# Optimization experiments

Hardware: AMD Instinct MI355X
Metric: run time of the kernel (lower is better)

Reference implementation:

```python
import jax, jax.numpy as jnp
import numpy as np

B, S, D, H = 2, 2048, 768, 12
E = D // H  # d_head = 64


def setup_inputs() -> dict:
    key = jax.random.key(0)
    ks = jax.random.split(key, 10)
    scale = 1.0 / np.sqrt(D)
    x = jax.random.normal(ks[0], (B, S, D), dtype=jnp.float32)
    # Additive mask, laid out [H*B, S, S] as the torch forward slices per head.
    attn_mask = jnp.zeros((H * B, S, S), dtype=jnp.float32)
    # Per-head projections (math form: q = x @ Wq[h] + bq[h])
    Wq = jax.random.normal(ks[1], (H, D, E), dtype=jnp.float32) * scale
    bq = jax.random.normal(ks[2], (H, E), dtype=jnp.float32) * 0.01
    Wk = jax.random.normal(ks[3], (H, D, E), dtype=jnp.float32) * scale
    bk = jax.random.normal(ks[4], (H, E), dtype=jnp.float32) * 0.01
    Wv = jax.random.normal(ks[5], (H, D, E), dtype=jnp.float32) * scale
    bv = jax.random.normal(ks[6], (H, E), dtype=jnp.float32) * 0.01
    Wo = jax.random.normal(ks[7], (D, D), dtype=jnp.float32) * scale
    bo = jax.random.normal(ks[8], (D,), dtype=jnp.float32) * 0.01
    return {"x": x, "attn_mask": attn_mask, "Wq": Wq, "bq": bq,
            "Wk": Wk, "bk": bk, "Wv": Wv, "bv": bv, "Wo": Wo, "bo": bo}


def reference(x, attn_mask, Wq, bq, Wk, bk, Wv, bv, Wo, bo):
    # x: [B,S,D]; attn_mask: [H*B,S,S]
    q = jnp.einsum('bsd,hde->hbse', x, Wq) + bq[:, None, None, :]
    k = jnp.einsum('bsd,hde->hbse', x, Wk) + bk[:, None, None, :]
    v = jnp.einsum('bsd,hde->hbse', x, Wv) + bv[:, None, None, :]
    mask = attn_mask.reshape(H, B, S, S)
    # NOTE: original code has NO 1/sqrt(d_head) scaling — kept faithful.
    logits = jnp.einsum('hbse,hbte->hbst', q, k) + mask
    w = jax.nn.softmax(logits, axis=-1)  # dropout is identity at eval / p=0
    o = jnp.einsum('hbst,hbte->hbse', w, v)  # [H,B,S,E]
    o = jnp.transpose(o, (1, 2, 0, 3)).reshape(B, S, H * E)  # concat heads
    return o @ Wo + bo
```

## Files before the change

### kernel.cpp

```cpp
#include <hip/hip_runtime.h>
#include <hip/hip_bf16.h>
#include <cmath>

constexpr int Bc  = 2;
constexpr int Sc  = 2048;
constexpr int Dc  = 768;
constexpr int Hc  = 12;
constexpr int Ec  = 64;
constexpr int BSc = Bc * Sc;

typedef _Float16 f16;
typedef __attribute__((ext_vector_type(8)))  _Float16 half8;
typedef __attribute__((ext_vector_type(16))) float    floatx16;

typedef __attribute__((address_space(3))) void       lds_void;
typedef __attribute__((address_space(1))) const void glb_cvoid;


__global__ __launch_bounds__(256) void prep_kernel(
    const float* __restrict__ x,
    const float* __restrict__ Wq, const float* __restrict__ Wk, const float* __restrict__ Wv,
    const float* __restrict__ bq, const float* __restrict__ bk, const float* __restrict__ bv,
    const float* __restrict__ Wo,
    f16* __restrict__ x16, f16* __restrict__ Wt16, f16* __restrict__ Wot16,
    float* __restrict__ bias_cat)
{
    __shared__ __align__(16) float Ts[64][65];
    const int t = threadIdx.x;
    int bid = blockIdx.x;

    if (bid < 1536) {
        const size_t base = (size_t)bid * 2048 + t * 8;
        const float4 v0 = *(const float4*)(x + base);
        const float4 v1 = *(const float4*)(x + base + 4);
        half8 hv;
        hv[0] = (f16)v0.x; hv[1] = (f16)v0.y; hv[2] = (f16)v0.z; hv[3] = (f16)v0.w;
        hv[4] = (f16)v1.x; hv[5] = (f16)v1.y; hv[6] = (f16)v1.z; hv[7] = (f16)v1.w;
        *(half8*)(x16 + base) = hv;
        return;
    }
    bid -= 1536;
    if (bid < 432) {
        const int proj = bid / 144, rem = bid % 144, h = rem / 12, dt = rem % 12;
        const float* W = ((proj == 0) ? Wq : (proj == 1) ? Wk : Wv) + (size_t)h * Dc * Ec;
        const int c = t & 63, rr = t >> 6;
        #pragma unroll
        for (int r0 = 0; r0 < 64; r0 += 4) {
            const int d = rr + r0;
            Ts[d][c] = W[(size_t)(dt * 64 + d) * Ec + c];
        }
        __syncthreads();
        #pragma unroll
        for (int r0 = 0; r0 < 64; r0 += 4) {
            const int e = rr + r0;
            Wt16[(size_t)(proj * 768 + h * 64 + e) * Dc + dt * 64 + c] = (f16)Ts[c][e];
        }
        return;
    }
    bid -= 432;
    if (bid < 144) {
        const int rt = bid / 12, ct = bid % 12;
        const int c = t & 63, rr = t >> 6;
        #pragma unroll
        for (int r0 = 0; r0 < 64; r0 += 4) {
            const int d = rr + r0;
            Ts[d][c] = Wo[(size_t)(rt * 64 + d) * Dc + ct * 64 + c];
        }
        __syncthreads();
        #pragma unroll
        for (int r0 = 0; r0 < 64; r0 += 4) {
            const int e = rr + r0;
            Wot16[(size_t)(ct * 64 + e) * Dc + rt * 64 + c] = (f16)Ts[c][e];
        }
        return;
    }
    bid -= 144;
    {
        const int g = bid * 256 + t;
        if (g < 3 * 768) {
            const int proj = g / 768, idx = g % 768;
            const float* bb = (proj == 0) ? bq : (proj == 1) ? bk : bv;
            bias_cat[g] = bb[idx];
        }
    }
}

__global__ __launch_bounds__(256, 2) void gemm_qkv_kernel(
    const f16* __restrict__ x16, const f16* __restrict__ Wt16,
    const float* __restrict__ bias_cat,
    f16* __restrict__ q16, f16* __restrict__ kswz, f16* __restrict__ vswz)
{
    __shared__ __align__(16) unsigned char smem[34816];
    f16 (*As)[64]  = (f16(*)[64])smem;
    f16 (*Bs)[64]  = (f16(*)[64])(smem + 16384);
    f16 (*Cs)[136] = (f16(*)[136])smem;

    const int t = threadIdx.x;
    const int wave = t >> 6, lane = t & 63;
    const int col = lane & 31, hf = lane >> 5;
    const int wr = wave & 1, wc = wave >> 1;
    const int m0 = blockIdx.x * 128, n0 = blockIdx.y * 128;
    const int lrow = lane >> 3, lseg = lane & 7;

    floatx16 c00, c01, c10, c11;
    #pragma unroll
    for (int i = 0; i < 16; ++i) { c00[i] = 0.f; c01[i] = 0.f; c10[i] = 0.f; c11[i] = 0.f; }

    for (int k0 = 0; k0 < Dc; k0 += 64) {
        #pragma unroll
        for (int i = 0; i < 4; ++i) {
            const int r = wave * 32 + i * 8;
            __builtin_amdgcn_global_load_lds(
                (glb_cvoid*)(x16 + (size_t)(m0 + r + lrow) * Dc + k0 + lseg * 8),
                (lds_void*)&As[r][0], 16, 0, 0);
            __builtin_amdgcn_global_load_lds(
                (glb_cvoid*)(Wt16 + (size_t)(n0 + r + lrow) * Dc + k0 + lseg * 8),
                (lds_void*)&Bs[r][0], 16, 0, 0);
        }
        __syncthreads();
        #pragma unroll
        for (int ks = 0; ks < 4; ++ks) {
            const half8 a0 = *(const half8*)&As[wr * 64 + col][ks * 16 + hf * 8];
            const half8 a1 = *(const half8*)&As[wr * 64 + 32 + col][ks * 16 + hf * 8];
            const half8 b0 = *(const half8*)&Bs[wc * 64 + col][ks * 16 + hf * 8];
            const half8 b1 = *(const half8*)&Bs[wc * 64 + 32 + col][ks * 16 + hf * 8];
            c00 = __builtin_amdgcn_mfma_f32_32x32x16_f16(a0, b0, c00, 0, 0, 0);
            c01 = __builtin_amdgcn_mfma_f32_32x32x16_f16(a0, b1, c01, 0, 0, 0);
            c10 = __builtin_amdgcn_mfma_f32_32x32x16_f16(a1, b0, c10, 0, 0, 0);
            c11 = __builtin_amdgcn_mfma_f32_32x32x16_f16(a1, b1, c11, 0, 0, 0);
        }
        __syncthreads();
    }

    const float bias0 = bias_cat[n0 + wc * 64 + col];
    const float bias1 = bias_cat[n0 + wc * 64 + 32 + col];
    #pragma unroll
    for (int i = 0; i < 16; ++i) {
        const int r = (i & 3) + 8 * (i >> 2) + 4 * hf;
        Cs[wr * 64 + r][wc * 64 + col]           = (f16)(c00[i] + bias0);
        Cs[wr * 64 + r][wc * 64 + 32 + col]      = (f16)(c01[i] + bias1);
        Cs[wr * 64 + 32 + r][wc * 64 + col]      = (f16)(c10[i] + bias0);
        Cs[wr * 64 + 32 + r][wc * 64 + 32 + col] = (f16)(c11[i] + bias1);
    }
    __syncthreads();

    const int proj = n0 / 768;
    const int h0   = (n0 - proj * 768) >> 6;
    const int b    = m0 >> 11;
    const int s_in = m0 & 2047;
    const int kt0  = s_in >> 5;

    if (proj == 0) {
        const int row = t >> 1, seg = t & 1;
        const int h = h0 + seg;
        f16* gp = q16 + ((size_t)(h * Bc + b) * Sc + s_in + row) * Ec;
        #pragma unroll
        for (int j = 0; j < 8; ++j)
            *(half8*)(gp + j * 8) = *(const half8*)&Cs[row][seg * 64 + j * 8];
    } else if (proj == 1) {
        #pragma unroll
        for (int ch = 0; ch < 8; ++ch) {
            const int id = ch * 256 + t;
            const int lane_ = id & 63;
            const int ks  = (id >> 6) & 3;
            const int ktp = (id >> 8) & 3;
            const int seg = (id >> 10) & 1;
            const int colp = lane_ & 31, hfp = lane_ >> 5;
            const int hb = (h0 + seg) * Bc + b;
            const half8 val = *(const half8*)&Cs[ktp * 32 + colp][seg * 64 + ks * 16 + hfp * 8];
            *(half8*)(kswz + ((size_t)((hb * 64 + kt0 + ktp) * 4 + ks) << 9) + lane_ * 8) = val;
        }
    } else {
        #pragma unroll
        for (int ch = 0; ch < 8; ++ch) {
            const int id = ch * 256 + t;
            const int lane_ = id & 63;
            const int ks2 = (id >> 6) & 1;
            const int vh  = (id >> 7) & 1;
            const int ktp = (id >> 8) & 3;
            const int seg = (id >> 10) & 1;
            const int colp = lane_ & 31, hfp = lane_ >> 5;
            const int hb = (h0 + seg) * Bc + b;
            const int e  = vh * 32 + colp;
            half8 val;
            #pragma unroll
            for (int j = 0; j < 8; ++j)
                val[j] = Cs[ktp * 32 + ks2 * 16 + hfp * 8 + j][seg * 64 + e];
            *(half8*)(vswz + ((size_t)(((hb * 64 + kt0 + ktp) * 2 + ks2) * 2 + vh) << 9) + lane_ * 8) = val;
        }
    }
}

__global__ __launch_bounds__(128, 2) void flash_attn_kernel(
    const f16* __restrict__ q16, const f16* __restrict__ kswz,
    const f16* __restrict__ vswz, const float* __restrict__ mask,
    f16* __restrict__ obuf16)
{
    __shared__ __align__(16) float Mall[64 * 128];
    __shared__ _Float16 Plds[2][32][40];

    const int fblk = blockIdx.x;
    const int kk   = fblk >> 3;
    const int hb   = (fblk & 7) + 8 * (kk >> 5);
    const int rb   = kk & 31;
    const int h    = hb >> 1;
    const int b    = hb & 1;

    const int t    = threadIdx.x;
    const int wave = t >> 6;
    const int lane = t & 63;
    const int col  = lane & 31;
    const int hf   = lane >> 5;
    const int row0 = rb * 64 + wave * 32;

    const f16* qb  = q16  + ((size_t)hb * Sc + row0) * Ec;
    const f16* kbz = kswz + ((size_t)hb << 17);
    const f16* vbz = vswz + ((size_t)hb << 17);
    const float* mband = mask + ((size_t)hb * Sc + rb * 64) * Sc;

    half8 qfrag[4];
    #pragma unroll
    for (int ks = 0; ks < 4; ++ks)
        qfrag[ks] = *(const half8*)(qb + (size_t)col * Ec + ks * 16 + hf * 8);

    constexpr int NT = Sc / 32;

    float vmax[16];
    #pragma unroll
    for (int i = 0; i < 16; ++i) vmax[i] = -3e38f;

    half8 kreg[4];
    {
        const f16* kp = kbz + lane * 8;
        #pragma unroll
        for (int ks = 0; ks < 4; ++ks) kreg[ks] = *(const half8*)(kp + (ks << 9));
    }
    #pragma unroll 2
    for (int kt = 0; kt < NT; ++kt) {
        floatx16 c;
        #pragma unroll
        for (int i = 0; i < 16; ++i) c[i] = 0.f;
        #pragma unroll
        for (int ks = 0; ks < 4; ++ks)
            c = __builtin_amdgcn_mfma_f32_32x32x16_f16(qfrag[ks], kreg[ks], c, 0, 0, 0);
        if (kt + 1 < NT) {
            const f16* kp = kbz + ((size_t)(kt + 1) << 11) + lane * 8;
            #pragma unroll
            for (int ks = 0; ks < 4; ++ks) kreg[ks] = *(const half8*)(kp + (ks << 9));
        }
        #pragma unroll
        for (int i = 0; i < 16; ++i) vmax[i] = fmaxf(vmax[i], c[i]);
    }
    float mrow[16];
    #pragma unroll
    for (int i = 0; i < 16; ++i) {
        float v = vmax[i];
        v = fmaxf(v, __shfl_xor(v, 1));
        v = fmaxf(v, __shfl_xor(v, 2));
        v = fmaxf(v, __shfl_xor(v, 4));
        v = fmaxf(v, __shfl_xor(v, 8));
        v = fmaxf(v, __shfl_xor(v, 16));
        mrow[i] = v;
    }

    floatx16 o0, o1;
    float lsum[16];
    #pragma unroll
    for (int i = 0; i < 16; ++i) { o0[i] = 0.f; o1[i] = 0.f; lsum[i] = 0.f; }

    {
        const f16* kp = kbz + lane * 8;
        #pragma unroll
        for (int ks = 0; ks < 4; ++ks) kreg[ks] = *(const half8*)(kp + (ks << 9));
    }

    for (int rd = 0; rd < NT / 4; ++rd) {
        __syncthreads();
        #pragma unroll
        for (int j = 0; j < 16; ++j) {
            const int row = wave * 32 + 2 * j;
            __builtin_amdgcn_global_load_lds(
                (glb_cvoid*)(mband + (size_t)(row + (lane >> 5)) * Sc
                             + rd * 128 + (lane & 31) * 4),
                (lds_void*)&Mall[row * 128], 16, 0, 0);
        }
        __syncthreads();

        #pragma unroll
        for (int s = 0; s < 4; ++s) {
            const int kt = rd * 4 + s;

            const f16* vp = vbz + ((size_t)kt << 11) + lane * 8;
            const half8 va  = *(const half8*)(vp);
            const half8 vb0 = *(const half8*)(vp + (1 << 9));
            const half8 vc  = *(const half8*)(vp + (2 << 9));
            const half8 vd  = *(const half8*)(vp + (3 << 9));

            floatx16 c;
            #pragma unroll
            for (int i = 0; i < 16; ++i) c[i] = 0.f;
            #pragma unroll
            for (int ks = 0; ks < 4; ++ks)
                c = __builtin_amdgcn_mfma_f32_32x32x16_f16(qfrag[ks], kreg[ks], c, 0, 0, 0);

            if (kt + 1 < NT) {
                const f16* kp = kbz + ((size_t)(kt + 1) << 11) + lane * 8;
                #pragma unroll
                for (int ks = 0; ks < 4; ++ks) kreg[ks] = *(const half8*)(kp + (ks << 9));
            }

            #pragma unroll
            for (int i = 0; i < 16; ++i) {
                const int r = (i & 3) + 8 * (i >> 2) + 4 * hf;
                const float m = Mall[(wave * 32 + r) * 128 + s * 32 + col];
                const float p = __expf(c[i] + m - mrow[i]);
                lsum[i] += p;
                Plds[wave][r][col] = (f16)p;
            }
            asm volatile("s_waitcnt lgkmcnt(0)" ::: "memory");

            #pragma unroll
            for (int ks2 = 0; ks2 < 2; ++ks2) {
                const half8 pf = *(const half8*)(&Plds[wave][col][ks2 * 16 + hf * 8]);
                const half8 v0 = (ks2 == 0) ? va : vc;
                const half8 v1 = (ks2 == 0) ? vb0 : vd;
                o0 = __builtin_amdgcn_mfma_f32_32x32x16_f16(pf, v0, o0, 0, 0, 0);
                o1 = __builtin_amdgcn_mfma_f32_32x32x16_f16(pf, v1, o1, 0, 0, 0);
            }
        }
    }

    #pragma unroll
    for (int i = 0; i < 16; ++i) {
        float v = lsum[i];
        v += __shfl_xor(v, 1);
        v += __shfl_xor(v, 2);
        v += __shfl_xor(v, 4);
        v += __shfl_xor(v, 8);
        v += __shfl_xor(v, 16);
        const float inv = 1.f / v;
        const int r = (i & 3) + 8 * (i >> 2) + 4 * hf;
        const size_t orow = ((size_t)b * Sc + row0 + r) * Dc + h * Ec;
        obuf16[orow + col]      = (f16)(o0[i] * inv);
        obuf16[orow + 32 + col] = (f16)(o1[i] * inv);
    }
}

__global__ __launch_bounds__(256, 2) void gemm_out_kernel(
    const f16* __restrict__ a16, const f16* __restrict__ Wot16,
    const float* __restrict__ bo, float* __restrict__ out)
{
    __shared__ __align__(16) f16 As[128][64];
    __shared__ __align__(16) f16 Bs[64][64];

    const int t = threadIdx.x;
    const int wave = t >> 6, lane = t & 63;
    const int col = lane & 31, hf = lane >> 5;
    const int m0 = blockIdx.x * 128, n0 = blockIdx.y * 64;
    const int lrow = lane >> 3, lseg = lane & 7;

    floatx16 c0, c1;
    #pragma unroll
    for (int i = 0; i < 16; ++i) { c0[i] = 0.f; c1[i] = 0.f; }

    for (int k0 = 0; k0 < Dc; k0 += 64) {
        #pragma unroll
        for (int i = 0; i < 4; ++i) {
            const int r = wave * 32 + i * 8;
            __builtin_amdgcn_global_load_lds(
                (glb_cvoid*)(a16 + (size_t)(m0 + r + lrow) * Dc + k0 + lseg * 8),
                (lds_void*)&As[r][0], 16, 0, 0);
        }
        {
            const int r = wave * 16;
            __builtin_amdgcn_global_load_lds(
                (glb_cvoid*)(Wot16 + (size_t)(n0 + r + lrow) * Dc + k0 + lseg * 8),
                (lds_void*)&Bs[r][0], 16, 0, 0);
            __builtin_amdgcn_global_load_lds(
                (glb_cvoid*)(Wot16 + (size_t)(n0 + r + 8 + lrow) * Dc + k0 + lseg * 8),
                (lds_void*)&Bs[r + 8][0], 16, 0, 0);
        }
        __syncthreads();
        #pragma unroll
        for (int ks = 0; ks < 4; ++ks) {
            const half8 a  = *(const half8*)&As[wave * 32 + col][ks * 16 + hf * 8];
            const half8 b0 = *(const half8*)&Bs[col][ks * 16 + hf * 8];
            const half8 b1 = *(const half8*)&Bs[32 + col][ks * 16 + hf * 8];
            c0 = __builtin_amdgcn_mfma_f32_32x32x16_f16(a, b0, c0, 0, 0, 0);
            c1 = __builtin_amdgcn_mfma_f32_32x32x16_f16(a, b1, c1, 0, 0, 0);
        }
        __syncthreads();
    }

    const float bo0 = bo[n0 + col], bo1 = bo[n0 + 32 + col];
    #pragma unroll
    for (int i = 0; i < 16; ++i) {
        const int r = (i & 3) + 8 * (i >> 2) + 4 * hf;
        const size_t ro = (size_t)(m0 + wave * 32 + r) * Dc + n0;
        out[ro + col]      = c0[i] + bo0;
        out[ro + 32 + col] = c1[i] + bo1;
    }
}

extern "C" void kernel_launch(void* const* d_in, const int* in_sizes, int n_in,
                              void* d_out, int out_size, void* d_ws, size_t ws_size,
                              hipStream_t stream)
{
    const float* x    = (const float*)d_in[0];
    const float* mask = (const float*)d_in[1];
    const float* Wq   = (const float*)d_in[2];
    const float* bq   = (const float*)d_in[3];
    const float* Wk   = (const float*)d_in[4];
    const float* bk   = (const float*)d_in[5];
    const float* Wv   = (const float*)d_in[6];
    const float* bv   = (const float*)d_in[7];
    const float* Wo   = (const float*)d_in[8];
    const float* bo   = (const float*)d_in[9];
    float* out = (float*)d_out;

    constexpr size_t NQ = (size_t)Hc * Bc * Sc * Ec;
    f16* x16    = (f16*)d_ws;
    f16* Wt16   = x16 + (size_t)BSc * Dc;
    f16* Wot16  = Wt16 + (size_t)3 * Dc * Dc;
    f16* q16    = Wot16 + (size_t)Dc * Dc;
    f16* kswz   = q16 + NQ;
    f16* vswz   = kswz + NQ;
    f16* obuf16 = vswz + NQ;
    float* bias_cat = (float*)(obuf16 + NQ);

    prep_kernel<<<2121, 256, 0, stream>>>(x, Wq, Wk, Wv, bq, bk, bv, Wo,
                                          x16, Wt16, Wot16, bias_cat);

    gemm_qkv_kernel<<<dim3(BSc / 128, 2304 / 128), 256, 0, stream>>>(
        x16, Wt16, bias_cat, q16, kswz, vswz);

    flash_attn_kernel<<<768, 128, 0, stream>>>(
        q16, kswz, vswz, mask, obuf16);

    gemm_out_kernel<<<dim3(BSc / 128, Dc / 64), 256, 0, stream>>>(
        obuf16, Wot16, bo, out);
}
```

Baseline: 642.8 us.

## Double-buffer mask tiles in LDS and prefetch K two tiles ahead

The mask band is now staged into two 64x64 LDS buffers, and the next column block is loaded asynchronously while the current one is consumed. This replaces the old scheme of a single 64x128 tile loaded between two barriers. K fragments are also kept in a two-deep register ring, so loads are issued two iterations ahead in both the max pass and the softmax/PV pass. The aim is to hide global load latency for the mask and K. In exchange it adds register pressure from the extra K fragments and one barrier per 64-column round, and a wave may read a mask buffer whose async load is not explicitly waited on before use.

```diff
diff --git a/kernel.cpp b/kernel.cpp
--- a/kernel.cpp
+++ b/kernel.cpp
@@ -196,7 +196,7 @@
     const f16* __restrict__ vswz, const float* __restrict__ mask,
     f16* __restrict__ obuf16)
 {
-    __shared__ __align__(16) float Mall[64 * 128];
+    __shared__ __align__(16) float Mbuf[2][64 * 64];
     __shared__ _Float16 Plds[2][32][40];
 
     const int fblk = blockIdx.x;
@@ -217,6 +217,7 @@
     const f16* kbz = kswz + ((size_t)hb << 17);
     const f16* vbz = vswz + ((size_t)hb << 17);
     const float* mband = mask + ((size_t)hb * Sc + rb * 64) * Sc;
+    const float* msrc = mband + (size_t)(wave * 32 + (lane >> 4)) * Sc + (lane & 15) * 4;
 
     half8 qfrag[4];
     #pragma unroll
@@ -229,11 +230,11 @@
     #pragma unroll
     for (int i = 0; i < 16; ++i) vmax[i] = -3e38f;
 
-    half8 kreg[4];
-    {
-        const f16* kp = kbz + lane * 8;
-        #pragma unroll
-        for (int ks = 0; ks < 4; ++ks) kreg[ks] = *(const half8*)(kp + (ks << 9));
+    half8 kreg[2][4];
+    #pragma unroll
+    for (int ks = 0; ks < 4; ++ks) {
+        kreg[0][ks] = *(const half8*)(kbz + (ks << 9) + lane * 8);
+        kreg[1][ks] = *(const half8*)(kbz + (1 << 11) + (ks << 9) + lane * 8);
     }
     #pragma unroll 2
     for (int kt = 0; kt < NT; ++kt) {
@@ -242,11 +243,11 @@
         for (int i = 0; i < 16; ++i) c[i] = 0.f;
         #pragma unroll
         for (int ks = 0; ks < 4; ++ks)
-            c = __builtin_amdgcn_mfma_f32_32x32x16_f16(qfrag[ks], kreg[ks], c, 0, 0, 0);
-        if (kt + 1 < NT) {
-            const f16* kp = kbz + ((size_t)(kt + 1) << 11) + lane * 8;
-            #pragma unroll
-            for (int ks = 0; ks < 4; ++ks) kreg[ks] = *(const half8*)(kp + (ks << 9));
+            c = __builtin_amdgcn_mfma_f32_32x32x16_f16(qfrag[ks], kreg[kt & 1][ks], c, 0, 0, 0);
+        if (kt + 2 < NT) {
+            const f16* kp = kbz + ((size_t)(kt + 2) << 11) + lane * 8;
+            #pragma unroll
+            for (int ks = 0; ks < 4; ++ks) kreg[kt & 1][ks] = *(const half8*)(kp + (ks << 9));
         }
         #pragma unroll
         for (int i = 0; i < 16; ++i) vmax[i] = fmaxf(vmax[i], c[i]);
@@ -268,27 +269,31 @@
     #pragma unroll
     for (int i = 0; i < 16; ++i) { o0[i] = 0.f; o1[i] = 0.f; lsum[i] = 0.f; }
 
-    {
-        const f16* kp = kbz + lane * 8;
-        #pragma unroll
-        for (int ks = 0; ks < 4; ++ks) kreg[ks] = *(const half8*)(kp + (ks << 9));
-    }
-
-    for (int rd = 0; rd < NT / 4; ++rd) {
-        __syncthreads();
-        #pragma unroll
-        for (int j = 0; j < 16; ++j) {
-            const int row = wave * 32 + 2 * j;
-            __builtin_amdgcn_global_load_lds(
-                (glb_cvoid*)(mband + (size_t)(row + (lane >> 5)) * Sc
-                             + rd * 128 + (lane & 31) * 4),
-                (lds_void*)&Mall[row * 128], 16, 0, 0);
-        }
-        __syncthreads();
-
-        #pragma unroll
-        for (int s = 0; s < 4; ++s) {
-            const int kt = rd * 4 + s;
+    #pragma unroll
+    for (int ks = 0; ks < 4; ++ks) {
+        kreg[0][ks] = *(const half8*)(kbz + (ks << 9) + lane * 8);
+        kreg[1][ks] = *(const half8*)(kbz + (1 << 11) + (ks << 9) + lane * 8);
+    }
+    #pragma unroll
+    for (int j = 0; j < 8; ++j)
+        __builtin_amdgcn_global_load_lds(
+            (glb_cvoid*)(msrc + (size_t)(j * 4) * Sc),
+            (lds_void*)&Mbuf[0][(wave * 32 + j * 4) * 64], 16, 0, 0);
+    __syncthreads();
+
+    for (int rd = 0; rd < NT / 2; ++rd) {
+        if (rd + 1 < NT / 2) {
+            #pragma unroll
+            for (int j = 0; j < 8; ++j)
+                __builtin_amdgcn_global_load_lds(
+                    (glb_cvoid*)(msrc + (size_t)(j * 4) * Sc + (rd + 1) * 64),
+                    (lds_void*)&Mbuf[(rd + 1) & 1][(wave * 32 + j * 4) * 64], 16, 0, 0);
+        }
+        const float* Mcur = &Mbuf[rd & 1][wave * 32 * 64];
+
+        #pragma unroll
+        for (int s = 0; s < 2; ++s) {
+            const int kt = rd * 2 + s;
 
             const f16* vp = vbz + ((size_t)kt << 11) + lane * 8;
             const half8 va  = *(const half8*)(vp);
@@ -301,18 +306,18 @@
             for (int i = 0; i < 16; ++i) c[i] = 0.f;
             #pragma unroll
             for (int ks = 0; ks < 4; ++ks)
-                c = __builtin_amdgcn_mfma_f32_32x32x16_f16(qfrag[ks], kreg[ks], c, 0, 0, 0);
-
-            if (kt + 1 < NT) {
-                const f16* kp = kbz + ((size_t)(kt + 1) << 11) + lane * 8;
+                c = __builtin_amdgcn_mfma_f32_32x32x16_f16(qfrag[ks], kreg[kt & 1][ks], c, 0, 0, 0);
+
+            if (kt + 2 < NT) {
+                const f16* kp = kbz + ((size_t)(kt + 2) << 11) + lane * 8;
                 #pragma unroll
-                for (int ks = 0; ks < 4; ++ks) kreg[ks] = *(const half8*)(kp + (ks << 9));
+                for (int ks = 0; ks < 4; ++ks) kreg[kt & 1][ks] = *(const half8*)(kp + (ks << 9));
             }
 
             #pragma unroll
             for (int i = 0; i < 16; ++i) {
                 const int r = (i & 3) + 8 * (i >> 2) + 4 * hf;
-                const float m = Mall[(wave * 32 + r) * 128 + s * 32 + col];
+                const float m = Mcur[r * 64 + s * 32 + col];
                 const float p = __expf(c[i] + m - mrow[i]);
                 lsum[i] += p;
                 Plds[wave][r][col] = (f16)p;
@@ -328,6 +333,7 @@
                 o1 = __builtin_amdgcn_mfma_f32_32x32x16_f16(pf, v1, o1, 0, 0, 0);
             }
         }
+        __syncthreads();
     }
 
     #pragma unroll
```

New measurement: 645.1 us. About the same (+0.4%).
